# Performance work log

Measured on AMD Instinct MI355X. Metric: run time of the kernel, lower is better.

The kernel has to match this reference:

```python
import jax, jax.numpy as jnp
import numpy as np

B, S, D, MAX_LEN = 4, 2048, 512, 2048
V = 2 * MAX_LEN + 1  # embedding table size
POS_MAX = 3000


def setup_inputs() -> dict:
    key = jax.random.key(0)
    k1, k2, k3 = jax.random.split(key, 3)
    x = jax.random.normal(k1, (B, S, D), dtype=jnp.float32)
    emb_table = jax.random.normal(k2, (V, D), dtype=jnp.float32) * 0.02
    positions = jnp.sort(jax.random.randint(k3, (B, S), 0, POS_MAX), axis=-1)
    return {"x": x, "emb_table": emb_table, "positions": positions}


def reference(x, emb_table, positions):
    # x: [B,S,D], emb_table: [2M+1, D], positions: [B,S] int
    Bc, Sc, _ = x.shape
    Vc = emb_table.shape[0]
    M = (Vc - 1) // 2
    # rel[b,i,j] = clamp(pos_i - pos_j, -M, M) + M   -> index into table
    rel = jnp.clip(positions[:, :, None] - positions[:, None, :], -M, M) + M  # [B,S,S]
    # mean_j emb[rel[b,i,j]] == (occurrence counts over V) @ table / S
    # counts[b,i,v] = #{j : rel[b,i,j] == v}; identical math, no [B,S,S,D] tensor.
    b_idx = jnp.arange(Bc)[:, None, None]
    i_idx = jnp.arange(Sc)[None, :, None]
    counts = jnp.zeros((Bc, Sc, Vc), dtype=x.dtype).at[b_idx, i_idx, rel].add(1.0)
    mean_emb = jnp.einsum('bsv,vd->bsd', counts, emb_table) / Sc  # [B,S,D]
    return x + mean_emb
```

## Files before the change

### kernel.cpp

```cpp
#include <hip/hip_runtime.h>
#include <hip/hip_bf16.h>
#include <cstdint>

#define NB 4
#define NS 2048
#define ND 512
#define NM 2048
#define NV 4097
#define NP 3000
#define RSW 3080
#define EBI_KB 129
#define HTI_BATCH_BYTES (2 * 256 * 1024)

typedef __bf16 bf16x8 __attribute__((ext_vector_type(8)));
typedef float f32x4 __attribute__((ext_vector_type(4)));

__device__ __forceinline__ unsigned short f2bf(float f) {
  union { __bf16 b; unsigned short u; } cv;
  cv.b = (__bf16)f;
  return cv.u;
}

__device__ __forceinline__ int lbound_dev(const int* a, int n, int key) {
  int lo = 0, hi = n;
  while (lo < hi) { int mid = (lo + hi) >> 1; if (a[mid] < key) lo = mid + 1; else hi = mid; }
  return lo;
}

__global__ void k1_hist(const int* __restrict__ pos, unsigned int* __restrict__ hist) {
  __shared__ unsigned int h[NP];
  int b = blockIdx.x, tid = threadIdx.x;
  for (int i = tid; i < NP; i += 256) h[i] = 0u;
  __syncthreads();
  const int* pb = pos + b * NS;
  for (int i = tid; i < NS; i += 256) atomicAdd(&h[pb[i]], 1u);
  __syncthreads();
  unsigned int* hb = hist + b * NP;
  for (int i = tid; i < NP; i += 256) hb[i] = h[i];
}

__global__ void k_prep(const int* __restrict__ pos, const unsigned int* __restrict__ hist,
                       const float* __restrict__ emb, unsigned short* __restrict__ HTI,
                       unsigned short* __restrict__ EBI, int* __restrict__ rs) {
  __shared__ float tile[64][65];
  int blk = blockIdx.x, tid = threadIdx.x;
  if (blk < 52) {
    int b = blk & 3, chunk = blk >> 2;
    int t = chunk * 256 + tid;
    if (t <= 3072) rs[b * RSW + t] = lbound_dev(pos + b * NS, NS, t);
    return;
  }
  if (blk < 564) {
    int idx = (blk - 52) * 256 + tid;
    int l = idx & 63;
    int tb = (idx >> 6) & 255;
    int p = (idx >> 14) & 1;
    int bb = idx >> 15;
    const unsigned int* hbt = hist + bb * NP;
    int base = 5104 + (l & 15) - tb * 32 - p * 16 - ((l >> 4) * 8);
    union { unsigned short us[8]; uint4 v4; } pk;
#pragma unroll
    for (int e = 0; e < 8; ++e) {
      int ii = base - e;
      float f = (ii >= 0 && ii < NP) ? (float)hbt[ii] : 0.0f;
      pk.us[e] = f2bf(f);
    }
    *(uint4*)(HTI + ((size_t)(bb * 2 + p) * 256 + tb) * 512 + l * 8) = pk.v4;
    return;
  }
  {
    int blk2 = blk - 564;
    int v0 = (blk2 % 65) * 64, d0 = (blk2 / 65) * 64;
    int c = tid & 63, r0 = tid >> 6;
#pragma unroll
    for (int k = 0; k < 16; ++k) {
      int r = k * 4 + r0;
      int v = v0 + r;
      float val = 0.f;
      if (v < NV && v != 0 && v != (NV - 1)) val = emb[(size_t)v * ND + d0 + c];
      tile[r][c] = val;
    }
    __syncthreads();
#pragma unroll
    for (int rep = 0; rep < 2; ++rep) {
      int tile_id = rep * 4 + (tid >> 6);
      int l = tid & 63;
      int kb_loc = tile_id >> 2, dt_loc = tile_id & 3;
      int kb = (v0 >> 5) + kb_loc, dt = (d0 >> 4) + dt_loc;
      if (kb < EBI_KB) {
        union { unsigned short us[8]; uint4 v4; } pk;
#pragma unroll
        for (int e = 0; e < 8; ++e)
          pk.us[e] = f2bf(tile[kb_loc * 32 + ((l >> 4) * 8) + e][dt_loc * 16 + (l & 15)]);
        *(uint4*)(EBI + ((size_t)dt * EBI_KB + kb) * 512 + l * 8) = pk.v4;
      }
    }
  }
}

#define LOADSET(sa0, sa1, sa2, sb0, sb1, sb2, sb3, tt)                              \
  if ((tt) < nt) {                                                                  \
    int tof = (tt) * 1024 + vo;                                                     \
    sa0 = *(const bf16x8*)(hb + (size_t)(cA0 + tof));                               \
    sa1 = *(const bf16x8*)(hb + (size_t)(cA1 + tof));                               \
    sa2 = *(const bf16x8*)(hb + (size_t)(cA2 + tof));                               \
    sb0 = *(const bf16x8*)(eb + (size_t)(cB0 + tof));                               \
    sb1 = *(const bf16x8*)(eb + (size_t)(cB1 + tof));                               \
    sb2 = *(const bf16x8*)(eb + (size_t)(cB2 + tof));                               \
    sb3 = *(const bf16x8*)(eb + (size_t)(cB3 + tof));                               \
  }

#define MMSET(sa0, sa1, sa2, sb0, sb1, sb2, sb3)                                    \
  acc[0][0] = __builtin_amdgcn_mfma_f32_16x16x32_bf16(sa0, sb0, acc[0][0], 0, 0, 0);\
  acc[0][1] = __builtin_amdgcn_mfma_f32_16x16x32_bf16(sa0, sb1, acc[0][1], 0, 0, 0);\
  acc[0][2] = __builtin_amdgcn_mfma_f32_16x16x32_bf16(sa0, sb2, acc[0][2], 0, 0, 0);\
  acc[0][3] = __builtin_amdgcn_mfma_f32_16x16x32_bf16(sa0, sb3, acc[0][3], 0, 0, 0);\
  acc[1][0] = __builtin_amdgcn_mfma_f32_16x16x32_bf16(sa1, sb0, acc[1][0], 0, 0, 0);\
  acc[1][1] = __builtin_amdgcn_mfma_f32_16x16x32_bf16(sa1, sb1, acc[1][1], 0, 0, 0);\
  acc[1][2] = __builtin_amdgcn_mfma_f32_16x16x32_bf16(sa1, sb2, acc[1][2], 0, 0, 0);\
  acc[1][3] = __builtin_amdgcn_mfma_f32_16x16x32_bf16(sa1, sb3, acc[1][3], 0, 0, 0);\
  acc[2][0] = __builtin_amdgcn_mfma_f32_16x16x32_bf16(sa2, sb0, acc[2][0], 0, 0, 0);\
  acc[2][1] = __builtin_amdgcn_mfma_f32_16x16x32_bf16(sa2, sb1, acc[2][1], 0, 0, 0);\
  acc[2][2] = __builtin_amdgcn_mfma_f32_16x16x32_bf16(sa2, sb2, acc[2][2], 0, 0, 0);\
  acc[2][3] = __builtin_amdgcn_mfma_f32_16x16x32_bf16(sa2, sb3, acc[2][3], 0, 0, 0);

__global__ __launch_bounds__(256)
void k4_gemm(const unsigned short* __restrict__ HTI, const unsigned short* __restrict__ EBI,
             const int* __restrict__ rs, const float* __restrict__ x,
             const float* __restrict__ emb, float* __restrict__ out) {
  int tid = threadIdx.x, w = tid >> 6, lane = tid & 63;
  int flat = (blockIdx.x & 7) * 64 + (blockIdx.x >> 3);
  int qb = flat & 31, db = (flat >> 5) & 3, b = flat >> 7;
  int Q0 = qb * 96, D0 = db * 128;
  int wm = w >> 1, wn = w & 1;
  int Qw = Q0 + wm * 48, Dw = D0 + wn * 64;

  int v_lo = (Q0 > 951) ? ((Q0 - 951) & ~31) : 0;
  int v_hi = Q0 + 2144; if (v_hi > 4128) v_hi = 4128;
  int nt = (v_hi - v_lo) >> 5;

  const char* hb = (const char*)HTI + (size_t)b * HTI_BATCH_BYTES;
  const char* eb = (const char*)EBI;

  int S0 = 3056 - Qw + v_lo;
  int S1 = S0 - 16, S2 = S0 - 32;
  int cA0 = (((S0 >> 4) & 1) * 256 + (S0 >> 5)) * 1024;
  int cA1 = (((S1 >> 4) & 1) * 256 + (S1 >> 5)) * 1024;
  int cA2 = (((S2 >> 4) & 1) * 256 + (S2 >> 5)) * 1024;
  int kb0 = v_lo >> 5, dt0 = Dw >> 4;
  int cB0 = ((dt0 + 0) * EBI_KB + kb0) * 1024;
  int cB1 = ((dt0 + 1) * EBI_KB + kb0) * 1024;
  int cB2 = ((dt0 + 2) * EBI_KB + kb0) * 1024;
  int cB3 = ((dt0 + 3) * EBI_KB + kb0) * 1024;
  int vo = lane * 16;

  f32x4 acc[3][4];
#pragma unroll
  for (int a1 = 0; a1 < 3; ++a1)
#pragma unroll
    for (int a2 = 0; a2 < 4; ++a2) { f32x4 z = {0.f, 0.f, 0.f, 0.f}; acc[a1][a2] = z; }

  bf16x8 a00, a01, a02, b00, b01, b02, b03;
  bf16x8 a10, a11, a12, b10, b11, b12, b13;
  bf16x8 a20, a21, a22, b20, b21, b22, b23;

  LOADSET(a00, a01, a02, b00, b01, b02, b03, 0);
  LOADSET(a10, a11, a12, b10, b11, b12, b13, 1);

  int t = 0;
  for (;;) {
    LOADSET(a20, a21, a22, b20, b21, b22, b23, t + 2);
    __builtin_amdgcn_s_barrier();
    MMSET(a00, a01, a02, b00, b01, b02, b03);
    if (++t == nt) break;
    LOADSET(a00, a01, a02, b00, b01, b02, b03, t + 2);
    __builtin_amdgcn_s_barrier();
    MMSET(a10, a11, a12, b10, b11, b12, b13);
    if (++t == nt) break;
    LOADSET(a10, a11, a12, b10, b11, b12, b13, t + 2);
    __builtin_amdgcn_s_barrier();
    MMSET(a20, a21, a22, b20, b21, b22, b23);
    if (++t == nt) break;
  }

  const int* rsb = rs + b * RSW;
  const float* xb = x + (size_t)b * NS * ND;
  float* outb = out + (size_t)b * NS * ND;
  int col = lane & 15, rb4 = (lane >> 4) * 4;
#pragma unroll
  for (int nf = 0; nf < 4; ++nf) {
    int dcol = Dw + nf * 16 + col;
    float e0v = emb[dcol];
    float eMv = emb[(size_t)(NV - 1) * ND + dcol];
#pragma unroll
    for (int mf = 0; mf < 3; ++mf) {
#pragma unroll
      for (int j = 0; j < 4; ++j) {
        int q = Qw + mf * 16 + rb4 + j;
        if (q >= NP) continue;
        int i0 = rsb[q], i1 = rsb[q + 1];
        if (i0 == i1) continue;
        int cge = (q >= NM) ? rsb[q - NM + 1] : 0;
        int cle = (q + NM < NP) ? (NS - rsb[q + NM]) : 0;
        float val = (acc[mf][nf][j] + (float)cge * eMv + (float)cle * e0v) * (1.0f / (float)NS);
        for (int i = i0; i < i1; ++i)
          outb[(size_t)i * ND + dcol] = xb[(size_t)i * ND + dcol] + val;
      }
    }
  }
}

extern "C" void kernel_launch(void* const* d_in, const int* in_sizes, int n_in,
                              void* d_out, int out_size, void* d_ws, size_t ws_size,
                              hipStream_t stream) {
  const float* x = (const float*)d_in[0];
  const float* emb = (const float*)d_in[1];
  const int* pos = (const int*)d_in[2];
  float* out = (float*)d_out;

  char* ws = (char*)d_ws;
  unsigned short* HTI = (unsigned short*)(ws);
  unsigned short* EBI = (unsigned short*)(ws + 2097152);
  unsigned int* hist = (unsigned int*)(ws + 6324224);
  int* rs = (int*)(ws + 6372224);

  hipLaunchKernelGGL(k1_hist, dim3(NB), dim3(256), 0, stream, pos, hist);
  hipLaunchKernelGGL(k_prep, dim3(1084), dim3(256), 0, stream, pos, hist, emb, HTI, EBI, rs);
  hipLaunchKernelGGL(k4_gemm, dim3(512), dim3(256), 0, stream, HTI, EBI, rs, x, emb, out);
}
```

Baseline: 169.9 us.

## Fuse histogram into prep kernel, retile GEMM per-wave, drop barriers

Drops the separate single-block-per-batch histogram kernel. Each HTI-building block now recomputes its batch's position histogram in shared memory, which removes one launch and a serialized low-parallelism stage at the cost of redundant histogram work in every block. The GEMM is retiled so each wave covers its own 48-row Q strip and all four waves share one 64-wide D slice. Each wave's V range is trimmed to its own strip, and the now-unneeded s_barriers in the main loop are removed.

```diff
diff --git a/kernel.cpp b/kernel.cpp
--- a/kernel.cpp
+++ b/kernel.cpp
@@ -27,22 +27,11 @@
   return lo;
 }
 
-__global__ void k1_hist(const int* __restrict__ pos, unsigned int* __restrict__ hist) {
+__global__ void k_prep(const int* __restrict__ pos, const float* __restrict__ emb,
+                       unsigned short* __restrict__ HTI, unsigned short* __restrict__ EBI,
+                       int* __restrict__ rs) {
+  __shared__ float tile[64][65];
   __shared__ unsigned int h[NP];
-  int b = blockIdx.x, tid = threadIdx.x;
-  for (int i = tid; i < NP; i += 256) h[i] = 0u;
-  __syncthreads();
-  const int* pb = pos + b * NS;
-  for (int i = tid; i < NS; i += 256) atomicAdd(&h[pb[i]], 1u);
-  __syncthreads();
-  unsigned int* hb = hist + b * NP;
-  for (int i = tid; i < NP; i += 256) hb[i] = h[i];
-}
-
-__global__ void k_prep(const int* __restrict__ pos, const unsigned int* __restrict__ hist,
-                       const float* __restrict__ emb, unsigned short* __restrict__ HTI,
-                       unsigned short* __restrict__ EBI, int* __restrict__ rs) {
-  __shared__ float tile[64][65];
   int blk = blockIdx.x, tid = threadIdx.x;
   if (blk < 52) {
     int b = blk & 3, chunk = blk >> 2;
@@ -52,17 +41,21 @@
   }
   if (blk < 564) {
     int idx = (blk - 52) * 256 + tid;
+    int bb = idx >> 15;
+    for (int i = tid; i < NP; i += 256) h[i] = 0u;
+    __syncthreads();
+    const int* pb = pos + bb * NS;
+    for (int i = tid; i < NS; i += 256) atomicAdd(&h[pb[i]], 1u);
+    __syncthreads();
     int l = idx & 63;
     int tb = (idx >> 6) & 255;
     int p = (idx >> 14) & 1;
-    int bb = idx >> 15;
-    const unsigned int* hbt = hist + bb * NP;
     int base = 5104 + (l & 15) - tb * 32 - p * 16 - ((l >> 4) * 8);
     union { unsigned short us[8]; uint4 v4; } pk;
 #pragma unroll
     for (int e = 0; e < 8; ++e) {
       int ii = base - e;
-      float f = (ii >= 0 && ii < NP) ? (float)hbt[ii] : 0.0f;
+      float f = (ii >= 0 && ii < NP) ? (float)h[ii] : 0.0f;
       pk.us[e] = f2bf(f);
     }
     *(uint4*)(HTI + ((size_t)(bb * 2 + p) * 256 + tb) * 512 + l * 8) = pk.v4;
@@ -130,24 +123,23 @@
              const float* __restrict__ emb, float* __restrict__ out) {
   int tid = threadIdx.x, w = tid >> 6, lane = tid & 63;
   int flat = (blockIdx.x & 7) * 64 + (blockIdx.x >> 3);
-  int qb = flat & 31, db = (flat >> 5) & 3, b = flat >> 7;
-  int Q0 = qb * 96, D0 = db * 128;
-  int wm = w >> 1, wn = w & 1;
-  int Qw = Q0 + wm * 48, Dw = D0 + wn * 64;
-
-  int v_lo = (Q0 > 951) ? ((Q0 - 951) & ~31) : 0;
-  int v_hi = Q0 + 2144; if (v_hi > 4128) v_hi = 4128;
+  int qb = flat & 15, db = (flat >> 4) & 7, b = flat >> 7;
+  int Q0w = qb * 192 + w * 48;
+  int D0w = db * 64;
+
+  int v_lo = (Q0w > 951) ? ((Q0w - 951) & ~31) : 0;
+  int v_hi = (Q0w + 2096 + 31) & ~31; if (v_hi > 4128) v_hi = 4128;
   int nt = (v_hi - v_lo) >> 5;
 
   const char* hb = (const char*)HTI + (size_t)b * HTI_BATCH_BYTES;
   const char* eb = (const char*)EBI;
 
-  int S0 = 3056 - Qw + v_lo;
+  int S0 = 3056 - Q0w + v_lo;
   int S1 = S0 - 16, S2 = S0 - 32;
   int cA0 = (((S0 >> 4) & 1) * 256 + (S0 >> 5)) * 1024;
   int cA1 = (((S1 >> 4) & 1) * 256 + (S1 >> 5)) * 1024;
   int cA2 = (((S2 >> 4) & 1) * 256 + (S2 >> 5)) * 1024;
-  int kb0 = v_lo >> 5, dt0 = Dw >> 4;
+  int kb0 = v_lo >> 5, dt0 = D0w >> 4;
   int cB0 = ((dt0 + 0) * EBI_KB + kb0) * 1024;
   int cB1 = ((dt0 + 1) * EBI_KB + kb0) * 1024;
   int cB2 = ((dt0 + 2) * EBI_KB + kb0) * 1024;
@@ -170,15 +162,12 @@
   int t = 0;
   for (;;) {
     LOADSET(a20, a21, a22, b20, b21, b22, b23, t + 2);
-    __builtin_amdgcn_s_barrier();
     MMSET(a00, a01, a02, b00, b01, b02, b03);
     if (++t == nt) break;
     LOADSET(a00, a01, a02, b00, b01, b02, b03, t + 2);
-    __builtin_amdgcn_s_barrier();
     MMSET(a10, a11, a12, b10, b11, b12, b13);
     if (++t == nt) break;
     LOADSET(a10, a11, a12, b10, b11, b12, b13, t + 2);
-    __builtin_amdgcn_s_barrier();
     MMSET(a20, a21, a22, b20, b21, b22, b23);
     if (++t == nt) break;
   }
@@ -189,14 +178,14 @@
   int col = lane & 15, rb4 = (lane >> 4) * 4;
 #pragma unroll
   for (int nf = 0; nf < 4; ++nf) {
-    int dcol = Dw + nf * 16 + col;
+    int dcol = D0w + nf * 16 + col;
     float e0v = emb[dcol];
     float eMv = emb[(size_t)(NV - 1) * ND + dcol];
 #pragma unroll
     for (int mf = 0; mf < 3; ++mf) {
 #pragma unroll
       for (int j = 0; j < 4; ++j) {
-        int q = Qw + mf * 16 + rb4 + j;
+        int q = Q0w + mf * 16 + rb4 + j;
         if (q >= NP) continue;
         int i0 = rsb[q], i1 = rsb[q + 1];
         if (i0 == i1) continue;
@@ -221,10 +210,8 @@
   char* ws = (char*)d_ws;
   unsigned short* HTI = (unsigned short*)(ws);
   unsigned short* EBI = (unsigned short*)(ws + 2097152);
-  unsigned int* hist = (unsigned int*)(ws + 6324224);
-  int* rs = (int*)(ws + 6372224);
-
-  hipLaunchKernelGGL(k1_hist, dim3(NB), dim3(256), 0, stream, pos, hist);
-  hipLaunchKernelGGL(k_prep, dim3(1084), dim3(256), 0, stream, pos, hist, emb, HTI, EBI, rs);
+  int* rs = (int*)(ws + 6324224);
+
+  hipLaunchKernelGGL(k_prep, dim3(1084), dim3(256), 0, stream, pos, emb, HTI, EBI, rs);
   hipLaunchKernelGGL(k4_gemm, dim3(512), dim3(256), 0, stream, HTI, EBI, rs, x, emb, out);
 }
```

Result: faster. 160.5 us (-5.6%).
